# Optimization experiments

Hardware: AMD Instinct MI355X
Metric: run time of the kernel (lower is better)

Reference implementation:

```python
import jax, jax.numpy as jnp
import numpy as np

B, N_AIM, N_DET, C = 4, 2048, 2048, 256  # inplanes=256, inter_channels=128


def _lin(x, w, b):
    # torch nn.Linear: y = x @ W^T + b, weight shape [out, in]
    return jnp.einsum('bnc,dc->bnd', x, w) + b


def setup_inputs() -> dict:
    key = jax.random.key(0)
    ks = jax.random.split(key, 16)
    s = 1.0 / np.sqrt(C)
    inp = {
        'detect': jax.random.normal(ks[0], (B, N_DET, C), jnp.float32),
        'aim': jax.random.normal(ks[1], (B, N_AIM, C), jnp.float32),
    }
    names = ['g', 'g2', 'theta', 'phi', 'W', 'Q']
    for i, nm in enumerate(names):
        inp[nm + '_w'] = jax.random.uniform(ks[2 + 2 * i], (C, C), jnp.float32, -s, s)
        inp[nm + '_b'] = jax.random.uniform(ks[3 + 2 * i], (C,), jnp.float32, -s, s)
    return inp


def reference(detect, aim, g_w, g_b, g2_w, g2_b, theta_w, theta_b, phi_w, phi_b, W_w, W_b, Q_w, Q_b):
    b, na, c = aim.shape
    nd = detect.shape[1]
    ic = c // 2  # inter_channels

    # view(B, ic, -1) on a contiguous [B, N, C] tensor -> row-major reshape to [B, ic, 2N]
    d_x = _lin(detect, g_w, g_b).reshape(b, ic, -1).transpose(0, 2, 1)      # (B, 2Nd, ic)
    a_x = _lin(aim, g2_w, g2_b).reshape(b, ic, -1).transpose(0, 2, 1)       # (B, 2Na, ic)
    theta_x = _lin(aim, theta_w, theta_b).reshape(b, ic, -1).transpose(0, 2, 1)  # (B, 2Na, ic)
    phi_x = _lin(detect, phi_w, phi_b).reshape(b, ic, -1)                   # (B, ic, 2Nd)

    f = jnp.matmul(theta_x, phi_x)                 # (B, 2Na, 2Nd)
    f_div_C = f / f.shape[-1]                      # scale by 2*Nd
    fi_div_C = jnp.swapaxes(f, 1, 2) / f.shape[-2] # (B, 2Nd, 2Na), scale by 2*Na

    non_aim = jnp.matmul(f_div_C, d_x)             # (B, 2Na, ic)
    non_aim = non_aim.transpose(0, 2, 1).reshape(b, na, c)
    non_aim = _lin(non_aim, W_w, W_b) + aim

    non_det = jnp.matmul(fi_div_C, a_x)            # (B, 2Nd, ic)
    non_det = non_det.transpose(0, 2, 1).reshape(b, nd, c)
    non_det = _lin(non_det, Q_w, Q_b) + detect

    return (non_det, non_aim)
```

## Files before the change

### kernel.cpp

```cpp
#include <hip/hip_runtime.h>


typedef __attribute__((ext_vector_type(4))) float  f32x4;
typedef __attribute__((ext_vector_type(8))) __bf16 bf16x8;
typedef __attribute__((ext_vector_type(8))) unsigned short u16x8;
typedef __attribute__((ext_vector_type(4))) unsigned short u16x4;

__device__ inline unsigned short f2bf(float f) {
    union { float f; unsigned u; } c; c.f = f;
    unsigned r = c.u + 0x7FFF + ((c.u >> 16) & 1);
    return (unsigned short)(r >> 16);
}
__device__ inline bf16x8 ldfrag(const unsigned short* p) {
    return __builtin_bit_cast(bf16x8, *(const u16x8*)p);
}

__global__ __launch_bounds__(256)
void lin4_kernel(const float* __restrict__ aim, const float* __restrict__ detect,
                 const float* __restrict__ g_w, const float* __restrict__ g2_w,
                 const float* __restrict__ th_w, const float* __restrict__ ph_w,
                 const float* __restrict__ b_g, const float* __restrict__ b_g2,
                 const float* __restrict__ b_th, const float* __restrict__ b_ph,
                 unsigned short* __restrict__ T,  unsigned short* __restrict__ Ga,
                 unsigned short* __restrict__ P,  unsigned short* __restrict__ Gd)
{
    const int bid = blockIdx.x, tid = threadIdx.x;
    const int lane = tid & 63, w = tid >> 6;
    const int wr = w >> 1, wc = w & 1, q = lane >> 4, ln = lane & 15;

    const int z = bid >> 8, rem = bid & 255, set = rem & 1, mtile = rem >> 1;
    const float* Ap = z ? detect : aim;
    const float* Wm = z ? (set ? g_w : ph_w) : (set ? g2_w : th_w);
    const float* Bv = z ? (set ? b_g : b_ph) : (set ? b_g2 : b_th);
    unsigned short* O = z ? (set ? Gd : P) : (set ? Ga : T);
    const int m0 = mtile * 64;

    __shared__ unsigned short As[64][40];
    __shared__ unsigned short Bs[256][40];

    f32x4 acc[2][8] = {};

    for (int k0 = 0; k0 < 256; k0 += 32) {
        #pragma unroll
        for (int i = 0; i < 2; ++i) {
            int idx = tid + i * 256, row = idx >> 3, c4 = idx & 7;
            float4 v = *(const float4*)(Ap + (size_t)(m0 + row) * 256 + k0 + c4 * 4);
            u16x4 p; p[0]=f2bf(v.x); p[1]=f2bf(v.y); p[2]=f2bf(v.z); p[3]=f2bf(v.w);
            *(u16x4*)&As[row][c4 * 4] = p;
        }
        #pragma unroll
        for (int i = 0; i < 8; ++i) {
            int idx = tid + i * 256, row = idx >> 3, c4 = idx & 7;
            float4 v = *(const float4*)(Wm + (size_t)row * 256 + k0 + c4 * 4);
            u16x4 p; p[0]=f2bf(v.x); p[1]=f2bf(v.y); p[2]=f2bf(v.z); p[3]=f2bf(v.w);
            *(u16x4*)&Bs[row][c4 * 4] = p;
        }
        __syncthreads();
        bf16x8 af[2], bb[8];
        #pragma unroll
        for (int i = 0; i < 2; ++i) af[i] = ldfrag(&As[wr * 32 + i * 16 + ln][q * 8]);
        #pragma unroll
        for (int j = 0; j < 8; ++j) bb[j] = ldfrag(&Bs[wc * 128 + j * 16 + ln][q * 8]);
        #pragma unroll
        for (int i = 0; i < 2; ++i)
            #pragma unroll
            for (int j = 0; j < 8; ++j)
                acc[i][j] = __builtin_amdgcn_mfma_f32_16x16x32_bf16(af[i], bb[j], acc[i][j], 0, 0, 0);
        __syncthreads();
    }

    #pragma unroll
    for (int i = 0; i < 2; ++i)
        #pragma unroll
        for (int j = 0; j < 8; ++j) {
            int n = wc * 128 + j * 16 + ln;
            float bias = Bv[n];
            #pragma unroll
            for (int r = 0; r < 4; ++r) {
                int m = m0 + wr * 32 + i * 16 + q * 4 + r;
                O[(size_t)m * 256 + n] = f2bf(acc[i][j][r] + bias);
            }
        }
}

__global__ __launch_bounds__(256)
void mid_kernel(const unsigned short* __restrict__ T, const unsigned short* __restrict__ P,
                const unsigned short* __restrict__ Gd, const unsigned short* __restrict__ Ga,
                const float* __restrict__ W_w, const float* __restrict__ Q_w,
                unsigned short* __restrict__ TW, unsigned short* __restrict__ PQ,
                float* __restrict__ S)
{
    __shared__ unsigned short lds[9216];

    const int tid = threadIdx.x, lane = tid & 63, w = tid >> 6;
    const int wr = w >> 1, wc = w & 1, q = lane >> 4, ln = lane & 15;

    if (blockIdx.x < 512) {
        const int bid = blockIdx.x;
        const int side = bid >> 8, rem = bid & 255, mtile = rem >> 1, nhalf = rem & 1;
        const unsigned short* Ap = side ? P : T;
        const float* Wm = side ? Q_w : W_w;
        unsigned short* O = side ? PQ : TW;
        const int m0 = mtile * 64, n0 = nhalf * 128;

        unsigned short (*As)[40] = (unsigned short (*)[40])lds;
        unsigned short (*Bs)[40] = (unsigned short (*)[40])(lds + 64 * 40);

        f32x4 acc[2][4] = {};

        for (int k0 = 0; k0 < 256; k0 += 32) {
            {
                int row = tid >> 2, c8 = tid & 3;
                *(u16x8*)&As[row][c8 * 8] = *(const u16x8*)(Ap + (size_t)(m0 + row) * 256 + k0 + c8 * 8);
            }
            #pragma unroll
            for (int i = 0; i < 4; ++i) {
                int idx = tid + i * 256, row = idx >> 3, c4 = idx & 7;
                float4 v = *(const float4*)(Wm + (size_t)(n0 + row) * 256 + k0 + c4 * 4);
                u16x4 p; p[0]=f2bf(v.x); p[1]=f2bf(v.y); p[2]=f2bf(v.z); p[3]=f2bf(v.w);
                *(u16x4*)&Bs[row][c4 * 4] = p;
            }
            __syncthreads();
            bf16x8 af[2], bb[4];
            #pragma unroll
            for (int i = 0; i < 2; ++i) af[i] = ldfrag(&As[wr * 32 + i * 16 + ln][q * 8]);
            #pragma unroll
            for (int j = 0; j < 4; ++j) bb[j] = ldfrag(&Bs[wc * 64 + j * 16 + ln][q * 8]);
            #pragma unroll
            for (int i = 0; i < 2; ++i)
                #pragma unroll
                for (int j = 0; j < 4; ++j)
                    acc[i][j] = __builtin_amdgcn_mfma_f32_16x16x32_bf16(af[i], bb[j], acc[i][j], 0, 0, 0);
            __syncthreads();
        }

        #pragma unroll
        for (int i = 0; i < 2; ++i)
            #pragma unroll
            for (int j = 0; j < 4; ++j) {
                int n = n0 + wc * 64 + j * 16 + ln;
                #pragma unroll
                for (int r = 0; r < 4; ++r) {
                    int m = m0 + wr * 32 + i * 16 + q * 4 + r;
                    O[(size_t)m * 256 + n] = f2bf(acc[i][j][r]);
                }
            }
    } else {
        const int bid = blockIdx.x - 512;
        const int which = bid >> 8, rem = bid & 255, batch = rem >> 6, rem2 = rem & 63;
        const int mt = rem2 >> 5, nt = (rem2 >> 4) & 1, chunk = rem2 & 15;
        const unsigned short* Ap = (which ? Ga : Gd) + (size_t)batch * 524288;
        const unsigned short* Bp = (which ? T  : P ) + (size_t)batch * 524288;
        float* Sp = S + ((size_t)(which * 4 + batch) << 14);
        const int kbeg = chunk * 256, m0 = mt * 64, n0 = nt * 64;

        unsigned short (*As)[72] = (unsigned short (*)[72])lds;
        unsigned short (*Bs)[72] = (unsigned short (*)[72])(lds + 64 * 72);

        f32x4 acc[2][2] = {};

        for (int kk = 0; kk < 4; ++kk) {
            const int k0 = kbeg + kk * 64;
            #pragma unroll
            for (int i = 0; i < 2; ++i) {
                int c = tid + i * 256, row = c >> 3, c8 = c & 7;
                *(u16x8*)&As[row][c8 * 8] = *(const u16x8*)(Ap + (size_t)(m0 + row) * 4096 + k0 + c8 * 8);
                *(u16x8*)&Bs[row][c8 * 8] = *(const u16x8*)(Bp + (size_t)(n0 + row) * 4096 + k0 + c8 * 8);
            }
            __syncthreads();
            #pragma unroll
            for (int ks = 0; ks < 2; ++ks) {
                bf16x8 af[2], bb[2];
                #pragma unroll
                for (int i = 0; i < 2; ++i) af[i] = ldfrag(&As[wr * 32 + i * 16 + ln][ks * 32 + q * 8]);
                #pragma unroll
                for (int j = 0; j < 2; ++j) bb[j] = ldfrag(&Bs[wc * 32 + j * 16 + ln][ks * 32 + q * 8]);
                #pragma unroll
                for (int i = 0; i < 2; ++i)
                    #pragma unroll
                    for (int j = 0; j < 2; ++j)
                        acc[i][j] = __builtin_amdgcn_mfma_f32_16x16x32_bf16(af[i], bb[j], acc[i][j], 0, 0, 0);
            }
            __syncthreads();
        }

        #pragma unroll
        for (int i = 0; i < 2; ++i)
            #pragma unroll
            for (int j = 0; j < 2; ++j)
                #pragma unroll
                for (int r = 0; r < 4; ++r) {
                    int m = m0 + wr * 32 + i * 16 + q * 4 + r, n = n0 + wc * 32 + j * 16 + ln;
                    unsafeAtomicAdd(Sp + m * 128 + n, acc[i][j][r]);
                }
    }
}

__global__ __launch_bounds__(256)
void combine_kernel(const float* __restrict__ S,
                    const unsigned short* __restrict__ TW, const unsigned short* __restrict__ PQ,
                    const float* __restrict__ W_b, const float* __restrict__ Q_b,
                    const float* __restrict__ aim, const float* __restrict__ detect,
                    float* __restrict__ out_aim, float* __restrict__ out_det)
{
    const int bid = blockIdx.x, tid = threadIdx.x;
    const int lane = tid & 63, w = tid >> 6;
    const int wr = w >> 1, wc = w & 1, q = lane >> 4, ln = lane & 15;

    const int which = bid >> 8, batch = (bid >> 6) & 3, qq = (bid >> 2) & 15;
    const int dtile = (bid >> 1) & 1, ihalf = bid & 1;
    const int d0 = dtile * 128, i0 = ihalf * 64;
    const float* Sm = S + ((size_t)(which * 4 + batch) << 14);
    const unsigned short* Bsrc = (which ? PQ : TW) + (size_t)batch * 524288;
    const float* Bv = which ? Q_b : W_b;
    const float* R  = (which ? detect : aim) + (size_t)batch * 524288;
    float* O = (which ? out_det : out_aim) + (size_t)batch * 524288;

    __shared__ unsigned short As[64][72];
    __shared__ unsigned short Bs[128][72];

    f32x4 acc[2][4] = {};

    for (int kk = 0; kk < 2; ++kk) {
        const int k0 = kk * 64;
        #pragma unroll
        for (int i = 0; i < 4; ++i) {
            int idx = tid + i * 256, row = idx >> 4, c4 = idx & 15;
            float4 v = *(const float4*)(Sm + (size_t)(i0 + row) * 128 + k0 + c4 * 4);
            u16x4 p;
            p[0]=f2bf(v.x * (1.0f/4096.0f)); p[1]=f2bf(v.y * (1.0f/4096.0f));
            p[2]=f2bf(v.z * (1.0f/4096.0f)); p[3]=f2bf(v.w * (1.0f/4096.0f));
            *(u16x4*)&As[row][c4 * 4] = p;
        }
        #pragma unroll
        for (int i = 0; i < 4; ++i) {
            int c = tid + i * 256, krow = c >> 4, dc = (c & 15) * 8;
            int gr = 16 * (k0 + krow) + qq;
            u16x8 v = *(const u16x8*)(Bsrc + (size_t)gr * 256 + d0 + dc);
            #pragma unroll
            for (int jj = 0; jj < 8; ++jj) Bs[dc + jj][krow] = v[jj];
        }
        __syncthreads();
        #pragma unroll
        for (int ks = 0; ks < 2; ++ks) {
            bf16x8 af[2], bb[4];
            #pragma unroll
            for (int i = 0; i < 2; ++i) af[i] = ldfrag(&As[wr * 32 + i * 16 + ln][ks * 32 + q * 8]);
            #pragma unroll
            for (int j = 0; j < 4; ++j) bb[j] = ldfrag(&Bs[wc * 64 + j * 16 + ln][ks * 32 + q * 8]);
            #pragma unroll
            for (int i = 0; i < 2; ++i)
                #pragma unroll
                for (int j = 0; j < 4; ++j)
                    acc[i][j] = __builtin_amdgcn_mfma_f32_16x16x32_bf16(af[i], bb[j], acc[i][j], 0, 0, 0);
        }
        __syncthreads();
    }

    #pragma unroll
    for (int i = 0; i < 2; ++i)
        #pragma unroll
        for (int j = 0; j < 4; ++j) {
            int d = d0 + wc * 64 + j * 16 + ln;
            float bias = Bv[d];
            #pragma unroll
            for (int r = 0; r < 4; ++r) {
                int iS = i0 + wr * 32 + i * 16 + q * 4 + r;
                size_t off = (size_t)(16 * iS + qq) * 256 + d;
                O[off] = acc[i][j][r] + bias + R[off];
            }
        }
}

extern "C" void kernel_launch(void* const* d_in, const int* in_sizes, int n_in,
                              void* d_out, int out_size, void* d_ws, size_t ws_size,
                              hipStream_t stream)
{
    const float* detect = (const float*)d_in[0];
    const float* aim    = (const float*)d_in[1];
    const float* g_w  = (const float*)d_in[2];  const float* g_b  = (const float*)d_in[3];
    const float* g2_w = (const float*)d_in[4];  const float* g2_b = (const float*)d_in[5];
    const float* th_w = (const float*)d_in[6];  const float* th_b = (const float*)d_in[7];
    const float* ph_w = (const float*)d_in[8];  const float* ph_b = (const float*)d_in[9];
    const float* W_w  = (const float*)d_in[10]; const float* W_b  = (const float*)d_in[11];
    const float* Q_w  = (const float*)d_in[12]; const float* Q_b  = (const float*)d_in[13];

    const size_t TOT = 8192L * 256;

    unsigned short* ws16 = (unsigned short*)d_ws;
    unsigned short* T   = ws16;
    unsigned short* P   = T  + TOT;
    unsigned short* Gd  = P  + TOT;
    unsigned short* Ga  = Gd + TOT;
    unsigned short* TW  = Ga + TOT;
    unsigned short* PQ  = TW + TOT;
    float* S    = (float*)(PQ + TOT);

    float* out_det = (float*)d_out;
    float* out_aim = out_det + TOT;

    hipMemsetAsync(S, 0, 131072 * 4, stream);
    lin4_kernel<<<dim3(512), 256, 0, stream>>>(
        aim, detect, g_w, g2_w, th_w, ph_w, g_b, g2_b, th_b, ph_b, T, Ga, P, Gd);
    mid_kernel<<<dim3(1024), 256, 0, stream>>>(T, P, Gd, Ga, W_w, Q_w, TW, PQ, S);
    combine_kernel<<<dim3(512), 256, 0, stream>>>(
        S, TW, PQ, W_b, Q_b, aim, detect, out_aim, out_det);
}
```

Before: 145.4 us.

## Precompose W·theta and Q·phi weights so TW/PQ come directly from inputs

Adds a small prep kernel that multiplies W_w by theta_w and Q_w by phi_w, and W_w by theta_b and Q_w by phi_b, producing fused weight matrices and bias vectors. The same prep kernel also zeroes the S accumulator, replacing the memset. The projection kernel now computes six linears directly from aim/detect in one launch, so TW and PQ no longer wait on T and P. This removes the serial dependency and the separate mid-kernel GEMM pass, but adds a fourth launch and a third bf16 rounding path for the composed weights.

```diff
diff --git a/kernel.cpp b/kernel.cpp
--- a/kernel.cpp
+++ b/kernel.cpp
@@ -16,23 +16,128 @@
 }
 
 __global__ __launch_bounds__(256)
-void lin4_kernel(const float* __restrict__ aim, const float* __restrict__ detect,
-                 const float* __restrict__ g_w, const float* __restrict__ g2_w,
+void prep_kernel(const float* __restrict__ W_w, const float* __restrict__ Q_w,
                  const float* __restrict__ th_w, const float* __restrict__ ph_w,
-                 const float* __restrict__ b_g, const float* __restrict__ b_g2,
-                 const float* __restrict__ b_th, const float* __restrict__ b_ph,
+                 const float* __restrict__ th_b, const float* __restrict__ ph_b,
+                 float* __restrict__ M1, float* __restrict__ M2,
+                 float* __restrict__ v1, float* __restrict__ v2,
+                 float* __restrict__ S)
+{
+    __shared__ unsigned short lds[7680];
+    const int bid = blockIdx.x, tid = threadIdx.x;
+
+    if (bid < 16) {
+        const int side = bid >> 3, rem = bid & 7, mtile = rem >> 1, nhalf = rem & 1;
+        const float* A  = side ? Q_w : W_w;
+        const float* Bm = side ? ph_w : th_w;
+        float* Mo = side ? M2 : M1;
+        const int m0 = mtile * 64, n0 = nhalf * 128;
+
+        unsigned short (*As)[40] = (unsigned short (*)[40])lds;
+        unsigned short (*Bs)[40] = (unsigned short (*)[40])(lds + 2560);
+
+        const int lane = tid & 63, w = tid >> 6;
+        const int wr = w >> 1, wc = w & 1, q = lane >> 4, ln = lane & 15;
+
+        f32x4 acc[2][4] = {};
+
+        for (int k0 = 0; k0 < 256; k0 += 32) {
+            #pragma unroll
+            for (int i = 0; i < 2; ++i) {
+                int idx = tid + i * 256, row = idx >> 3, c4 = idx & 7;
+                float4 v = *(const float4*)(A + (size_t)(m0 + row) * 256 + k0 + c4 * 4);
+                u16x4 p; p[0]=f2bf(v.x); p[1]=f2bf(v.y); p[2]=f2bf(v.z); p[3]=f2bf(v.w);
+                *(u16x4*)&As[row][c4 * 4] = p;
+            }
+            #pragma unroll
+            for (int i = 0; i < 4; ++i) {
+                int idx = tid + i * 256, dr = idx >> 5, c4 = idx & 31;
+                float4 v = *(const float4*)(Bm + (size_t)(k0 + dr) * 256 + n0 + c4 * 4);
+                Bs[c4 * 4 + 0][dr] = f2bf(v.x); Bs[c4 * 4 + 1][dr] = f2bf(v.y);
+                Bs[c4 * 4 + 2][dr] = f2bf(v.z); Bs[c4 * 4 + 3][dr] = f2bf(v.w);
+            }
+            __syncthreads();
+            bf16x8 af[2], bb[4];
+            #pragma unroll
+            for (int i = 0; i < 2; ++i) af[i] = ldfrag(&As[wr * 32 + i * 16 + ln][q * 8]);
+            #pragma unroll
+            for (int j = 0; j < 4; ++j) bb[j] = ldfrag(&Bs[wc * 64 + j * 16 + ln][q * 8]);
+            #pragma unroll
+            for (int i = 0; i < 2; ++i)
+                #pragma unroll
+                for (int j = 0; j < 4; ++j)
+                    acc[i][j] = __builtin_amdgcn_mfma_f32_16x16x32_bf16(af[i], bb[j], acc[i][j], 0, 0, 0);
+            __syncthreads();
+        }
+
+        #pragma unroll
+        for (int i = 0; i < 2; ++i)
+            #pragma unroll
+            for (int j = 0; j < 4; ++j) {
+                int n = n0 + wc * 64 + j * 16 + ln;
+                #pragma unroll
+                for (int r = 0; r < 4; ++r) {
+                    int m = m0 + wr * 32 + i * 16 + q * 4 + r;
+                    Mo[(size_t)m * 256 + n] = acc[i][j][r];
+                }
+            }
+    } else if (bid < 18) {
+        const int side = bid - 16;
+        const float* Wsrc = side ? Q_w : W_w;
+        const float* bsrc = side ? ph_b : th_b;
+        float* vout = side ? v2 : v1;
+        float* bs = (float*)lds;
+        if (tid < 64) *(float4*)(bs + tid * 4) = *(const float4*)(bsrc + tid * 4);
+        __syncthreads();
+        const int g = tid >> 2, sub = tid & 3;
+        #pragma unroll
+        for (int p = 0; p < 4; ++p) {
+            int e = p * 64 + g;
+            float s = 0.f;
+            #pragma unroll
+            for (int jj = 0; jj < 16; ++jj) {
+                float4 v = *(const float4*)(Wsrc + (size_t)e * 256 + sub * 64 + jj * 4);
+                int b0 = sub * 64 + jj * 4;
+                s += v.x * bs[b0] + v.y * bs[b0 + 1] + v.z * bs[b0 + 2] + v.w * bs[b0 + 3];
+            }
+            s += __shfl_xor(s, 1); s += __shfl_xor(s, 2);
+            if (sub == 0) vout[e] = s;
+        }
+    } else {
+        const int b = bid - 18;
+        float4 z = {0.f, 0.f, 0.f, 0.f};
+        #pragma unroll
+        for (int i = 0; i < 8; ++i)
+            ((float4*)S)[(size_t)b * 2048 + tid + i * 256] = z;
+    }
+}
+
+__global__ __launch_bounds__(256)
+void lin6_kernel(const float* __restrict__ aim, const float* __restrict__ detect,
+                 const float* __restrict__ th_w, const float* __restrict__ g2_w,
+                 const float* __restrict__ ph_w, const float* __restrict__ g_w,
+                 const float* __restrict__ th_b, const float* __restrict__ g2_b,
+                 const float* __restrict__ ph_b, const float* __restrict__ g_b,
+                 const float* __restrict__ M1, const float* __restrict__ M2,
+                 const float* __restrict__ v1, const float* __restrict__ v2,
                  unsigned short* __restrict__ T,  unsigned short* __restrict__ Ga,
-                 unsigned short* __restrict__ P,  unsigned short* __restrict__ Gd)
+                 unsigned short* __restrict__ TW, unsigned short* __restrict__ P,
+                 unsigned short* __restrict__ Gd, unsigned short* __restrict__ PQ)
 {
     const int bid = blockIdx.x, tid = threadIdx.x;
     const int lane = tid & 63, w = tid >> 6;
     const int wr = w >> 1, wc = w & 1, q = lane >> 4, ln = lane & 15;
 
-    const int z = bid >> 8, rem = bid & 255, set = rem & 1, mtile = rem >> 1;
-    const float* Ap = z ? detect : aim;
-    const float* Wm = z ? (set ? g_w : ph_w) : (set ? g2_w : th_w);
-    const float* Bv = z ? (set ? b_g : b_ph) : (set ? b_g2 : b_th);
-    unsigned short* O = z ? (set ? Gd : P) : (set ? Ga : T);
+    const int mat = bid >> 7, mtile = bid & 127;
+    const float* Ap; const float* Wm; const float* Bv; unsigned short* O;
+    switch (mat) {
+        case 0:  Ap = aim;    Wm = th_w; Bv = th_b; O = T;  break;
+        case 1:  Ap = aim;    Wm = g2_w; Bv = g2_b; O = Ga; break;
+        case 2:  Ap = aim;    Wm = M1;   Bv = v1;   O = TW; break;
+        case 3:  Ap = detect; Wm = ph_w; Bv = ph_b; O = P;  break;
+        case 4:  Ap = detect; Wm = g_w;  Bv = g_b;  O = Gd; break;
+        default: Ap = detect; Wm = M2;   Bv = v2;   O = PQ; break;
+    }
     const int m0 = mtile * 64;
 
     __shared__ unsigned short As[64][40];
@@ -84,116 +189,60 @@
 }
 
 __global__ __launch_bounds__(256)
-void mid_kernel(const unsigned short* __restrict__ T, const unsigned short* __restrict__ P,
-                const unsigned short* __restrict__ Gd, const unsigned short* __restrict__ Ga,
-                const float* __restrict__ W_w, const float* __restrict__ Q_w,
-                unsigned short* __restrict__ TW, unsigned short* __restrict__ PQ,
-                float* __restrict__ S)
-{
-    __shared__ unsigned short lds[9216];
-
-    const int tid = threadIdx.x, lane = tid & 63, w = tid >> 6;
+void spart_kernel(const unsigned short* __restrict__ T, const unsigned short* __restrict__ P,
+                  const unsigned short* __restrict__ Gd, const unsigned short* __restrict__ Ga,
+                  float* __restrict__ S)
+{
+    const int bid = blockIdx.x, tid = threadIdx.x;
+    const int lane = tid & 63, w = tid >> 6;
     const int wr = w >> 1, wc = w & 1, q = lane >> 4, ln = lane & 15;
 
-    if (blockIdx.x < 512) {
-        const int bid = blockIdx.x;
-        const int side = bid >> 8, rem = bid & 255, mtile = rem >> 1, nhalf = rem & 1;
-        const unsigned short* Ap = side ? P : T;
-        const float* Wm = side ? Q_w : W_w;
-        unsigned short* O = side ? PQ : TW;
-        const int m0 = mtile * 64, n0 = nhalf * 128;
-
-        unsigned short (*As)[40] = (unsigned short (*)[40])lds;
-        unsigned short (*Bs)[40] = (unsigned short (*)[40])(lds + 64 * 40);
-
-        f32x4 acc[2][4] = {};
-
-        for (int k0 = 0; k0 < 256; k0 += 32) {
-            {
-                int row = tid >> 2, c8 = tid & 3;
-                *(u16x8*)&As[row][c8 * 8] = *(const u16x8*)(Ap + (size_t)(m0 + row) * 256 + k0 + c8 * 8);
-            }
-            #pragma unroll
-            for (int i = 0; i < 4; ++i) {
-                int idx = tid + i * 256, row = idx >> 3, c4 = idx & 7;
-                float4 v = *(const float4*)(Wm + (size_t)(n0 + row) * 256 + k0 + c4 * 4);
-                u16x4 p; p[0]=f2bf(v.x); p[1]=f2bf(v.y); p[2]=f2bf(v.z); p[3]=f2bf(v.w);
-                *(u16x4*)&Bs[row][c4 * 4] = p;
-            }
-            __syncthreads();
-            bf16x8 af[2], bb[4];
-            #pragma unroll
-            for (int i = 0; i < 2; ++i) af[i] = ldfrag(&As[wr * 32 + i * 16 + ln][q * 8]);
-            #pragma unroll
-            for (int j = 0; j < 4; ++j) bb[j] = ldfrag(&Bs[wc * 64 + j * 16 + ln][q * 8]);
+    const int which = bid >> 8, rem = bid & 255, batch = rem >> 6, rem2 = rem & 63;
+    const int mt = rem2 >> 5, nt = (rem2 >> 4) & 1, chunk = rem2 & 15;
+    const unsigned short* Ap = (which ? Ga : Gd) + (size_t)batch * 524288;
+    const unsigned short* Bp = (which ? T  : P ) + (size_t)batch * 524288;
+    float* Sp = S + ((size_t)(which * 4 + batch) << 14);
+    const int kbeg = chunk * 256, m0 = mt * 64, n0 = nt * 64;
+
+    __shared__ unsigned short As[64][72];
+    __shared__ unsigned short Bs[64][72];
+
+    f32x4 acc[2][2] = {};
+
+    for (int kk = 0; kk < 4; ++kk) {
+        const int k0 = kbeg + kk * 64;
+        #pragma unroll
+        for (int i = 0; i < 2; ++i) {
+            int c = tid + i * 256, row = c >> 3, c8 = c & 7;
+            *(u16x8*)&As[row][c8 * 8] = *(const u16x8*)(Ap + (size_t)(m0 + row) * 4096 + k0 + c8 * 8);
+            *(u16x8*)&Bs[row][c8 * 8] = *(const u16x8*)(Bp + (size_t)(n0 + row) * 4096 + k0 + c8 * 8);
+        }
+        __syncthreads();
+        #pragma unroll
+        for (int ks = 0; ks < 2; ++ks) {
+            bf16x8 af[2], bb[2];
+            #pragma unroll
+            for (int i = 0; i < 2; ++i) af[i] = ldfrag(&As[wr * 32 + i * 16 + ln][ks * 32 + q * 8]);
+            #pragma unroll
+            for (int j = 0; j < 2; ++j) bb[j] = ldfrag(&Bs[wc * 32 + j * 16 + ln][ks * 32 + q * 8]);
             #pragma unroll
             for (int i = 0; i < 2; ++i)
                 #pragma unroll
-                for (int j = 0; j < 4; ++j)
+                for (int j = 0; j < 2; ++j)
                     acc[i][j] = __builtin_amdgcn_mfma_f32_16x16x32_bf16(af[i], bb[j], acc[i][j], 0, 0, 0);
-            __syncthreads();
-        }
-
-        #pragma unroll
-        for (int i = 0; i < 2; ++i)
-            #pragma unroll
-            for (int j = 0; j < 4; ++j) {
-                int n = n0 + wc * 64 + j * 16 + ln;
-                #pragma unroll
-                for (int r = 0; r < 4; ++r) {
-                    int m = m0 + wr * 32 + i * 16 + q * 4 + r;
-                    O[(size_t)m * 256 + n] = f2bf(acc[i][j][r]);
-                }
-            }
-    } else {
-        const int bid = blockIdx.x - 512;
-        const int which = bid >> 8, rem = bid & 255, batch = rem >> 6, rem2 = rem & 63;
-        const int mt = rem2 >> 5, nt = (rem2 >> 4) & 1, chunk = rem2 & 15;
-        const unsigned short* Ap = (which ? Ga : Gd) + (size_t)batch * 524288;
-        const unsigned short* Bp = (which ? T  : P ) + (size_t)batch * 524288;
-        float* Sp = S + ((size_t)(which * 4 + batch) << 14);
-        const int kbeg = chunk * 256, m0 = mt * 64, n0 = nt * 64;
-
-        unsigned short (*As)[72] = (unsigned short (*)[72])lds;
-        unsigned short (*Bs)[72] = (unsigned short (*)[72])(lds + 64 * 72);
-
-        f32x4 acc[2][2] = {};
-
-        for (int kk = 0; kk < 4; ++kk) {
-            const int k0 = kbeg + kk * 64;
-            #pragma unroll
-            for (int i = 0; i < 2; ++i) {
-                int c = tid + i * 256, row = c >> 3, c8 = c & 7;
-                *(u16x8*)&As[row][c8 * 8] = *(const u16x8*)(Ap + (size_t)(m0 + row) * 4096 + k0 + c8 * 8);
-                *(u16x8*)&Bs[row][c8 * 8] = *(const u16x8*)(Bp + (size_t)(n0 + row) * 4096 + k0 + c8 * 8);
-            }
-            __syncthreads();
-            #pragma unroll
-            for (int ks = 0; ks < 2; ++ks) {
-                bf16x8 af[2], bb[2];
-                #pragma unroll
-                for (int i = 0; i < 2; ++i) af[i] = ldfrag(&As[wr * 32 + i * 16 + ln][ks * 32 + q * 8]);
-                #pragma unroll
-                for (int j = 0; j < 2; ++j) bb[j] = ldfrag(&Bs[wc * 32 + j * 16 + ln][ks * 32 + q * 8]);
-                #pragma unroll
-                for (int i = 0; i < 2; ++i)
-                    #pragma unroll
-                    for (int j = 0; j < 2; ++j)
-                        acc[i][j] = __builtin_amdgcn_mfma_f32_16x16x32_bf16(af[i], bb[j], acc[i][j], 0, 0, 0);
-            }
-            __syncthreads();
-        }
-
-        #pragma unroll
-        for (int i = 0; i < 2; ++i)
-            #pragma unroll
-            for (int j = 0; j < 2; ++j)
-                #pragma unroll
-                for (int r = 0; r < 4; ++r) {
-                    int m = m0 + wr * 32 + i * 16 + q * 4 + r, n = n0 + wc * 32 + j * 16 + ln;
-                    unsafeAtomicAdd(Sp + m * 128 + n, acc[i][j][r]);
-                }
-    }
+        }
+        __syncthreads();
+    }
+
+    #pragma unroll
+    for (int i = 0; i < 2; ++i)
+        #pragma unroll
+        for (int j = 0; j < 2; ++j)
+            #pragma unroll
+            for (int r = 0; r < 4; ++r) {
+                int m = m0 + wr * 32 + i * 16 + q * 4 + r, n = n0 + wc * 32 + j * 16 + ln;
+                unsafeAtomicAdd(Sp + m * 128 + n, acc[i][j][r]);
+            }
 }
 
 __global__ __launch_bounds__(256)
@@ -295,14 +344,20 @@
     unsigned short* TW  = Ga + TOT;
     unsigned short* PQ  = TW + TOT;
     float* S    = (float*)(PQ + TOT);
+    float* M1   = S + 131072;
+    float* M2   = M1 + 65536;
+    float* v1   = M2 + 65536;
+    float* v2   = v1 + 256;
 
     float* out_det = (float*)d_out;
     float* out_aim = out_det + TOT;
 
-    hipMemsetAsync(S, 0, 131072 * 4, stream);
-    lin4_kernel<<<dim3(512), 256, 0, stream>>>(
-        aim, detect, g_w, g2_w, th_w, ph_w, g_b, g2_b, th_b, ph_b, T, Ga, P, Gd);
-    mid_kernel<<<dim3(1024), 256, 0, stream>>>(T, P, Gd, Ga, W_w, Q_w, TW, PQ, S);
+    prep_kernel<<<dim3(34), 256, 0, stream>>>(
+        W_w, Q_w, th_w, ph_w, th_b, ph_b, M1, M2, v1, v2, S);
+    lin6_kernel<<<dim3(768), 256, 0, stream>>>(
+        aim, detect, th_w, g2_w, ph_w, g_w, th_b, g2_b, ph_b, g_b,
+        M1, M2, v1, v2, T, Ga, TW, P, Gd, PQ);
+    spart_kernel<<<dim3(512), 256, 0, stream>>>(T, P, Gd, Ga, S);
     combine_kernel<<<dim3(512), 256, 0, stream>>>(
         S, TW, PQ, W_b, Q_b, aim, detect, out_aim, out_det);
 }
```

Measured after the change: 166.6 us. +14.6%, slower.
